# Kernel tuning notes

Measured on AMD Instinct MI355X. Metric: run time of the kernel, lower is better.

The kernel has to match this reference:

```python
import jax, jax.numpy as jnp
import numpy as np

HIDDEN = 128

def setup_inputs() -> dict:
    key = jax.random.key(0)
    ks = jax.random.split(key, 4)
    B, T, D, H = 64, 2048, 64, HIDDEN
    scale_ih = 1.0 / np.sqrt(D)
    scale_hh = 1.0 / np.sqrt(H)
    return {
        "input_data": jax.random.normal(ks[0], (B, T, D), dtype=jnp.float32),
        "W_ih": jax.random.normal(ks[1], (4 * H, D), dtype=jnp.float32) * scale_ih,
        "W_hh": jax.random.normal(ks[2], (4 * H, H), dtype=jnp.float32) * scale_hh,
        "b_ih": jnp.zeros((4 * H,), dtype=jnp.float32),
        "b_hh": jnp.zeros((4 * H,), dtype=jnp.float32),
        "h0": jnp.zeros((B, H), dtype=jnp.float32),
        "c0": jnp.zeros((B, H), dtype=jnp.float32),
    }

def reference(input_data, W_ih, W_hh, b_ih, b_hh, h0, c0):
    # Single-layer LSTM over the sequence, PyTorch gate order (i, f, g, o).
    H = h0.shape[-1]
    b = b_ih + b_hh  # (4H,)
    # Precompute input projections for all timesteps: (T, B, 4H)
    x_proj = jnp.einsum('btd,gd->tbg', input_data, W_ih) + b

    def step(carry, xp_t):
        h, c = carry  # (B, H) each
        gates = xp_t + h @ W_hh.T  # (B, 4H)
        i = jax.nn.sigmoid(gates[:, 0 * H:1 * H])
        f = jax.nn.sigmoid(gates[:, 1 * H:2 * H])
        g = jnp.tanh(gates[:, 2 * H:3 * H])
        o = jax.nn.sigmoid(gates[:, 3 * H:4 * H])
        c_new = f * c + i * g
        h_new = o * jnp.tanh(c_new)
        return (h_new, c_new), h_new

    (_, _), hs = jax.lax.scan(step, (h0, c0), x_proj)  # hs: (T, B, H)
    input_encoded = jnp.transpose(hs, (1, 0, 2))  # (B, T, H)
    return input_encoded
```

## Files before the change

### kernel.cpp

```cpp
#include <hip/hip_runtime.h>

typedef _Float16 half2f __attribute__((ext_vector_type(2)));

#define HID 128
#define G4  512
#define DIN 64

__device__ __forceinline__ float fdot2(half2f a, half2f b, float c) {
  return __builtin_amdgcn_fdot2(a, b, c, false);
}
__device__ __forceinline__ half2f as_h2(unsigned int u) {
  return __builtin_bit_cast(half2f, u);
}
__device__ __forceinline__ half2f mk2(float a, float b) {
  half2f r; r.x = (_Float16)a; r.y = (_Float16)b; return r;
}
__device__ __forceinline__ float sigmoidf_fast(float x) {
  return __builtin_amdgcn_rcpf(1.0f + __expf(-x));
}
__device__ __forceinline__ float tanhf_fast(float x) {
  return 2.0f * __builtin_amdgcn_rcpf(1.0f + __expf(-2.0f * x)) - 1.0f;
}
template <int CTRL>
__device__ __forceinline__ float dpp_add(float x) {
  int m = __builtin_amdgcn_update_dpp(0, __builtin_bit_cast(int, x),
                                      CTRL, 0xF, 0xF, true);
  return x + __builtin_bit_cast(float, m);
}
#define QP_XOR1 0xB1

__device__ __forceinline__ void barrier_lgkm() {
  asm volatile("s_waitcnt lgkmcnt(0)" ::: "memory");
  __builtin_amdgcn_s_barrier();
  asm volatile("" ::: "memory");
}

__global__ __launch_bounds__(512, 2)
void xproj_kernel(const float* __restrict__ x, const float* __restrict__ Wih,
                  const float* __restrict__ bih, const float* __restrict__ bhh,
                  _Float16* __restrict__ xp, int nrows)
{
  const int gp   = threadIdx.x;
  const int unit = gp >> 2;
  const int gate = gp & 3;
  const int row  = gate * HID + unit;

  half2f wi[32];
  {
    const float4* wr = (const float4*)(Wih + (size_t)row * DIN);
#pragma unroll
    for (int q = 0; q < 16; q++) {
      float4 v = wr[q];
      wi[2 * q + 0] = mk2(v.x, v.y);
      wi[2 * q + 1] = mk2(v.z, v.w);
    }
  }
  const float bias = bih[row] + bhh[row];

  __shared__ __align__(16) _Float16 xin[8 * DIN];

  const int rows_per_block = (nrows + (int)gridDim.x - 1) / (int)gridDim.x;
  const int r0 = blockIdx.x * rows_per_block;
  const int r1 = (r0 + rows_per_block < nrows) ? (r0 + rows_per_block) : nrows;

  const int rsub = threadIdx.x >> 6;
  const int dd   = threadIdx.x & 63;

  float vld = 0.f;
  if (r0 + rsub < nrows) vld = x[(size_t)(r0 + rsub) * DIN + dd];

  for (int r = r0; r < r1; r += 8) {
    barrier_lgkm();
    xin[rsub * DIN + dd] = (_Float16)vld;
    barrier_lgkm();
    int rn = r + 8 + rsub;
    if (rn < nrows) vld = x[(size_t)rn * DIN + dd];

    const uint4* xi4 = (const uint4*)xin;
#pragma unroll
    for (int k = 0; k < 8; k++) {
      if (r + k >= r1) break;
      const uint4* rowp = xi4 + k * (DIN / 8);
      float a[4] = {bias, 0.f, 0.f, 0.f};
#pragma unroll
      for (int q = 0; q < 8; q++) {
        uint4 hv = rowp[q];
        a[q & 3] = fdot2(as_h2(hv.x), wi[4 * q + 0], a[q & 3]);
        a[q & 3] = fdot2(as_h2(hv.y), wi[4 * q + 1], a[q & 3]);
        a[q & 3] = fdot2(as_h2(hv.z), wi[4 * q + 2], a[q & 3]);
        a[q & 3] = fdot2(as_h2(hv.w), wi[4 * q + 3], a[q & 3]);
      }
      xp[(size_t)(r + k) * G4 + gp] = (_Float16)(a[0] + a[1] + a[2] + a[3]);
    }
  }
}

__global__ __launch_bounds__(256, 1)
void lstm_scan5(const float* __restrict__ Whh,
                const float* __restrict__ h0, const float* __restrict__ c0,
                const _Float16* __restrict__ xp,
                float* __restrict__ out, int T)
{
  const int tid = threadIdx.x;
  const int j   = tid >> 1;
  const int kq  = tid & 1;
  const int b   = blockIdx.x;

  half2f w0[32], w1[32], w2[32], w3[32];
  {
    const float4* r0 = (const float4*)(Whh + ((size_t)(0 * HID + j)) * HID + kq * 64);
    const float4* r1 = (const float4*)(Whh + ((size_t)(1 * HID + j)) * HID + kq * 64);
    const float4* r2 = (const float4*)(Whh + ((size_t)(2 * HID + j)) * HID + kq * 64);
    const float4* r3 = (const float4*)(Whh + ((size_t)(3 * HID + j)) * HID + kq * 64);
#pragma unroll
    for (int q = 0; q < 16; q++) {
      float4 v;
      v = r0[q]; w0[2 * q] = mk2(v.x, v.y); w0[2 * q + 1] = mk2(v.z, v.w);
      v = r1[q]; w1[2 * q] = mk2(v.x, v.y); w1[2 * q + 1] = mk2(v.z, v.w);
      v = r2[q]; w2[2 * q] = mk2(v.x, v.y); w2[2 * q + 1] = mk2(v.z, v.w);
      v = r3[q]; w3[2 * q] = mk2(v.x, v.y); w3[2 * q + 1] = mk2(v.z, v.w);
    }
  }

  __shared__ __align__(16) _Float16 h_sh[2][HID];

  float c = c0[(size_t)b * HID + j];
  if (kq == 0) h_sh[0][j] = (_Float16)h0[(size_t)b * HID + j];
  __syncthreads();

  const unsigned int* xp32 = (const unsigned int*)xp;
  const size_t xbase = (size_t)b * T * 256 + (size_t)j * 2 + kq;
  unsigned int xv  = xp32[xbase];
  unsigned int xv1 = (T > 1) ? xp32[xbase + 256] : 0u;

  const _Float16* rb = h_sh[0];
  _Float16*       wb = h_sh[1];

  for (int t = 0; t < T; ++t) {
    unsigned int xv2 = 0;
    if (t + 2 < T) xv2 = xp32[xbase + (size_t)(t + 2) * 256];

    uint4 hv[8];
    const uint4* h4 = (const uint4*)(rb + kq * 64);
#pragma unroll
    for (int q = 0; q < 8; q++) hv[q] = h4[q];

    float a0 = 0.f, a1 = 0.f, a2 = 0.f, a3 = 0.f;
#pragma unroll
    for (int q = 0; q < 8; q++) {
      unsigned int d0 = hv[q].x, d1 = hv[q].y, d2 = hv[q].z, d3 = hv[q].w;
      a0 = fdot2(as_h2(d0), w0[4 * q + 0], a0);
      a1 = fdot2(as_h2(d0), w1[4 * q + 0], a1);
      a2 = fdot2(as_h2(d0), w2[4 * q + 0], a2);
      a3 = fdot2(as_h2(d0), w3[4 * q + 0], a3);
      a0 = fdot2(as_h2(d1), w0[4 * q + 1], a0);
      a1 = fdot2(as_h2(d1), w1[4 * q + 1], a1);
      a2 = fdot2(as_h2(d1), w2[4 * q + 1], a2);
      a3 = fdot2(as_h2(d1), w3[4 * q + 1], a3);
      a0 = fdot2(as_h2(d2), w0[4 * q + 2], a0);
      a1 = fdot2(as_h2(d2), w1[4 * q + 2], a1);
      a2 = fdot2(as_h2(d2), w2[4 * q + 2], a2);
      a3 = fdot2(as_h2(d2), w3[4 * q + 2], a3);
      a0 = fdot2(as_h2(d3), w0[4 * q + 3], a0);
      a1 = fdot2(as_h2(d3), w1[4 * q + 3], a1);
      a2 = fdot2(as_h2(d3), w2[4 * q + 3], a2);
      a3 = fdot2(as_h2(d3), w3[4 * q + 3], a3);
    }

    {
      half2f xh = as_h2(xv);
      float x0 = (float)xh.x, x1 = (float)xh.y;
      if (kq == 0) { a0 += x0; a1 += x1; }
      else         { a2 += x0; a3 += x1; }
    }

    a0 = dpp_add<QP_XOR1>(a0);
    a1 = dpp_add<QP_XOR1>(a1);
    a2 = dpp_add<QP_XOR1>(a2);
    a3 = dpp_add<QP_XOR1>(a3);

    float i  = sigmoidf_fast(a0);
    float f  = sigmoidf_fast(a1);
    float gg = tanhf_fast(a2);
    float o  = sigmoidf_fast(a3);
    c = f * c + i * gg;
    float h = o * tanhf_fast(c);

    if (kq == 0) {
      wb[j] = (_Float16)h;
      out[((size_t)b * T + t) * HID + j] = h;
    }
    barrier_lgkm();
    const _Float16* tmp = rb; rb = wb; wb = (_Float16*)tmp;
    xv = xv1; xv1 = xv2;
  }
}

__global__ __launch_bounds__(512, 2)
void lstm_scan_fb(const float* __restrict__ x, const float* __restrict__ Wih,
                  const float* __restrict__ Whh,
                  const float* __restrict__ bih, const float* __restrict__ bhh,
                  const float* __restrict__ h0, const float* __restrict__ c0,
                  float* __restrict__ out, int T)
{
  const int g = threadIdx.x;
  const int b = blockIdx.x;

  half2f w[64];
  {
    const float4* wr = (const float4*)(Whh + (size_t)g * HID);
#pragma unroll
    for (int q = 0; q < 32; q++) {
      float4 v = wr[q];
      w[2 * q + 0] = mk2(v.x, v.y);
      w[2 * q + 1] = mk2(v.z, v.w);
    }
  }
  half2f wi[32];
  float bias;
  {
    const float4* wr = (const float4*)(Wih + (size_t)g * DIN);
#pragma unroll
    for (int q = 0; q < 16; q++) {
      float4 v = wr[q];
      wi[2 * q + 0] = mk2(v.x, v.y);
      wi[2 * q + 1] = mk2(v.z, v.w);
    }
    bias = bih[g] + bhh[g];
  }

  __shared__ __align__(16) _Float16 h_sh[HID];
  __shared__ __align__(16) _Float16 xin[DIN];
  __shared__ float pre[G4];

  float c = 0.f;
  if (g < HID) {
    c = c0[(size_t)b * HID + g];
    h_sh[g] = (_Float16)h0[(size_t)b * HID + g];
  }
  if (g < DIN) xin[g] = (_Float16)x[((size_t)b * T) * DIN + g];
  __syncthreads();

  const bool is_tanh_gate = (g >= 2 * HID) && (g < 3 * HID);

  for (int t = 0; t < T; ++t) {
    float a[4] = {0.f, 0.f, 0.f, 0.f};
    const uint4* h4 = (const uint4*)h_sh;
#pragma unroll
    for (int q = 0; q < 16; q++) {
      uint4 hv = h4[q];
      a[q & 3] = fdot2(as_h2(hv.x), w[4 * q + 0], a[q & 3]);
      a[q & 3] = fdot2(as_h2(hv.y), w[4 * q + 1], a[q & 3]);
      a[q & 3] = fdot2(as_h2(hv.z), w[4 * q + 2], a[q & 3]);
      a[q & 3] = fdot2(as_h2(hv.w), w[4 * q + 3], a[q & 3]);
    }
    const uint4* x4 = (const uint4*)xin;
#pragma unroll
    for (int q = 0; q < 8; q++) {
      uint4 hv = x4[q];
      a[q & 3] = fdot2(as_h2(hv.x), wi[4 * q + 0], a[q & 3]);
      a[q & 3] = fdot2(as_h2(hv.y), wi[4 * q + 1], a[q & 3]);
      a[q & 3] = fdot2(as_h2(hv.z), wi[4 * q + 2], a[q & 3]);
      a[q & 3] = fdot2(as_h2(hv.w), wi[4 * q + 3], a[q & 3]);
    }
    float preact = a[0] + a[1] + a[2] + a[3] + bias;
    float act = is_tanh_gate ? tanhf_fast(preact) : sigmoidf_fast(preact);
    pre[g] = act;
    __syncthreads();

    if (g < HID) {
      float i  = pre[g];
      float f  = pre[g + HID];
      float gg = pre[g + 2 * HID];
      float o  = pre[g + 3 * HID];
      c = f * c + i * gg;
      float h = o * tanhf_fast(c);
      out[((size_t)b * T + t) * HID + g] = h;
      h_sh[g] = (_Float16)h;
    } else if (g >= HID && g < HID + DIN) {
      int d = g - HID;
      if (t + 1 < T) xin[d] = (_Float16)x[((size_t)b * T + (t + 1)) * DIN + d];
    }
    __syncthreads();
  }
}

extern "C" void kernel_launch(void* const* d_in, const int* in_sizes, int n_in,
                              void* d_out, int out_size, void* d_ws, size_t ws_size,
                              hipStream_t stream)
{
  const float* x   = (const float*)d_in[0];
  const float* Wih = (const float*)d_in[1];
  const float* Whh = (const float*)d_in[2];
  const float* bih = (const float*)d_in[3];
  const float* bhh = (const float*)d_in[4];
  const float* h0  = (const float*)d_in[5];
  const float* c0  = (const float*)d_in[6];
  float* out = (float*)d_out;

  const int B = in_sizes[5] / HID;
  const int T = in_sizes[0] / (B * DIN);
  const int nrows = B * T;

  const size_t xp_bytes = (size_t)nrows * G4 * sizeof(_Float16);
  if (ws_size >= xp_bytes) {
    _Float16* xp = (_Float16*)d_ws;
    xproj_kernel<<<1024, 512, 0, stream>>>(x, Wih, bih, bhh, xp, nrows);
    lstm_scan5<<<B, 256, 0, stream>>>(Whh, h0, c0, xp, out, T);
  } else {
    lstm_scan_fb<<<B, 512, 0, stream>>>(x, Wih, Whh, bih, bhh, h0, c0, out, T);
  }
}
```

Before: 1.092 ms.

## Use MFMA 16x16x32 for recurrent matvec with permuted x-projection layout

The per-timestep h·W_hh^T product, previously done with fdot2 per thread, now runs on MFMA 16x16x32 f16 instructions. Each wave holds W_hh fragments in registers, and the x-projection is written in a permuted order so one uint4 load per lane seeds the accumulators. Gate activations are computed per lane with a unified sigmoid/tanh formula and broadcast with DPP quad permutes. The MFMA uses only one useful row of the 16-row A tile, so most of its work is wasted; this shortens the serial dependency chain per step in exchange for that waste and a more complex lane mapping.

```diff
diff --git a/kernel.cpp b/kernel.cpp
--- a/kernel.cpp
+++ b/kernel.cpp
@@ -1,6 +1,8 @@
 #include <hip/hip_runtime.h>
 
 typedef _Float16 half2f __attribute__((ext_vector_type(2)));
+typedef _Float16 half8  __attribute__((ext_vector_type(8)));
+typedef float    floatx4 __attribute__((ext_vector_type(4)));
 
 #define HID 128
 #define G4  512
@@ -15,6 +17,14 @@
 __device__ __forceinline__ half2f mk2(float a, float b) {
   half2f r; r.x = (_Float16)a; r.y = (_Float16)b; return r;
 }
+__device__ __forceinline__ half8 cvt8(float4 a, float4 b) {
+  half8 r;
+  r[0] = (_Float16)a.x; r[1] = (_Float16)a.y;
+  r[2] = (_Float16)a.z; r[3] = (_Float16)a.w;
+  r[4] = (_Float16)b.x; r[5] = (_Float16)b.y;
+  r[6] = (_Float16)b.z; r[7] = (_Float16)b.w;
+  return r;
+}
 __device__ __forceinline__ float sigmoidf_fast(float x) {
   return __builtin_amdgcn_rcpf(1.0f + __expf(-x));
 }
@@ -22,12 +32,15 @@
   return 2.0f * __builtin_amdgcn_rcpf(1.0f + __expf(-2.0f * x)) - 1.0f;
 }
 template <int CTRL>
-__device__ __forceinline__ float dpp_add(float x) {
+__device__ __forceinline__ float dpp_bcast(float x) {
   int m = __builtin_amdgcn_update_dpp(0, __builtin_bit_cast(int, x),
                                       CTRL, 0xF, 0xF, true);
-  return x + __builtin_bit_cast(float, m);
-}
-#define QP_XOR1 0xB1
+  return __builtin_bit_cast(float, m);
+}
+#define QP_B0 0x00
+#define QP_B1 0x55
+#define QP_B2 0xAA
+#define QP_B3 0xFF
 
 __device__ __forceinline__ void barrier_lgkm() {
   asm volatile("s_waitcnt lgkmcnt(0)" ::: "memory");
@@ -44,6 +57,7 @@
   const int unit = gp >> 2;
   const int gate = gp & 3;
   const int row  = gate * HID + unit;
+  const int sidx = ((gp >> 7) << 7) + ((gp & 15) << 3) + ((gp >> 4) & 7);
 
   half2f wi[32];
   {
@@ -90,109 +104,129 @@
         a[q & 3] = fdot2(as_h2(hv.z), wi[4 * q + 2], a[q & 3]);
         a[q & 3] = fdot2(as_h2(hv.w), wi[4 * q + 3], a[q & 3]);
       }
-      xp[(size_t)(r + k) * G4 + gp] = (_Float16)(a[0] + a[1] + a[2] + a[3]);
+      xp[(size_t)(r + k) * G4 + sidx] = (_Float16)(a[0] + a[1] + a[2] + a[3]);
     }
   }
 }
 
 __global__ __launch_bounds__(256, 1)
-void lstm_scan5(const float* __restrict__ Whh,
+void lstm_scan6(const float* __restrict__ Whh,
                 const float* __restrict__ h0, const float* __restrict__ c0,
                 const _Float16* __restrict__ xp,
                 float* __restrict__ out, int T)
 {
-  const int tid = threadIdx.x;
-  const int j   = tid >> 1;
-  const int kq  = tid & 1;
-  const int b   = blockIdx.x;
-
-  half2f w0[32], w1[32], w2[32], w3[32];
-  {
-    const float4* r0 = (const float4*)(Whh + ((size_t)(0 * HID + j)) * HID + kq * 64);
-    const float4* r1 = (const float4*)(Whh + ((size_t)(1 * HID + j)) * HID + kq * 64);
-    const float4* r2 = (const float4*)(Whh + ((size_t)(2 * HID + j)) * HID + kq * 64);
-    const float4* r3 = (const float4*)(Whh + ((size_t)(3 * HID + j)) * HID + kq * 64);
-#pragma unroll
-    for (int q = 0; q < 16; q++) {
-      float4 v;
-      v = r0[q]; w0[2 * q] = mk2(v.x, v.y); w0[2 * q + 1] = mk2(v.z, v.w);
-      v = r1[q]; w1[2 * q] = mk2(v.x, v.y); w1[2 * q + 1] = mk2(v.z, v.w);
-      v = r2[q]; w2[2 * q] = mk2(v.x, v.y); w2[2 * q + 1] = mk2(v.z, v.w);
-      v = r3[q]; w3[2 * q] = mk2(v.x, v.y); w3[2 * q + 1] = mk2(v.z, v.w);
-    }
-  }
+  const int tid  = threadIdx.x;
+  const int w    = tid >> 6;
+  const int lane = tid & 63;
+  const int s    = lane >> 4;
+  const int col  = lane & 15;
+  const int gt   = lane & 3;
+  const int b    = blockIdx.x;
+
+  half8 bfr[8][4];
+#pragma unroll
+  for (int ti = 0; ti < 8; ti++) {
+    const int G    = (w * 8 + ti) * 16 + col;
+    const int unit = G >> 2;
+    const int g_   = G & 3;
+    const float* wrow = Whh + (size_t)(g_ * HID + unit) * HID;
+#pragma unroll
+    for (int kc = 0; kc < 4; kc++) {
+      const float4* p = (const float4*)(wrow + kc * 32 + s * 8);
+      bfr[ti][kc] = cvt8(p[0], p[1]);
+    }
+  }
+
+  const float kk = (gt == 2) ? -2.f : -1.f;
+  const float mm = (gt == 2) ?  2.f :  1.f;
+  const float bb = (gt == 2) ? -1.f :  0.f;
+
+  const int u0 = w * 32 + s * 8 + (col >> 2);
+  const int u1 = u0 + 4;
 
   __shared__ __align__(16) _Float16 h_sh[2][HID];
 
-  float c = c0[(size_t)b * HID + j];
-  if (kq == 0) h_sh[0][j] = (_Float16)h0[(size_t)b * HID + j];
-  __syncthreads();
-
-  const unsigned int* xp32 = (const unsigned int*)xp;
-  const size_t xbase = (size_t)b * T * 256 + (size_t)j * 2 + kq;
-  unsigned int xv  = xp32[xbase];
-  unsigned int xv1 = (T > 1) ? xp32[xbase + 256] : 0u;
+  float cA = c0[(size_t)b * HID + u0];
+  float cB = c0[(size_t)b * HID + u1];
+  if (tid < HID) h_sh[0][tid] = (_Float16)h0[(size_t)b * HID + tid];
+
+  const uint4* xp4 = (const uint4*)xp;
+  const size_t xbase = (size_t)b * T * (G4 / 8) + w * 16 + col;
+  uint4 xq  = xp4[xbase];
+  uint4 xq1 = (T > 1) ? xp4[xbase + 64] : xq;
+
+  barrier_lgkm();
 
   const _Float16* rb = h_sh[0];
   _Float16*       wb = h_sh[1];
 
   for (int t = 0; t < T; ++t) {
-    unsigned int xv2 = 0;
-    if (t + 2 < T) xv2 = xp32[xbase + (size_t)(t + 2) * 256];
-
-    uint4 hv[8];
-    const uint4* h4 = (const uint4*)(rb + kq * 64);
-#pragma unroll
-    for (int q = 0; q < 8; q++) hv[q] = h4[q];
-
-    float a0 = 0.f, a1 = 0.f, a2 = 0.f, a3 = 0.f;
-#pragma unroll
-    for (int q = 0; q < 8; q++) {
-      unsigned int d0 = hv[q].x, d1 = hv[q].y, d2 = hv[q].z, d3 = hv[q].w;
-      a0 = fdot2(as_h2(d0), w0[4 * q + 0], a0);
-      a1 = fdot2(as_h2(d0), w1[4 * q + 0], a1);
-      a2 = fdot2(as_h2(d0), w2[4 * q + 0], a2);
-      a3 = fdot2(as_h2(d0), w3[4 * q + 0], a3);
-      a0 = fdot2(as_h2(d1), w0[4 * q + 1], a0);
-      a1 = fdot2(as_h2(d1), w1[4 * q + 1], a1);
-      a2 = fdot2(as_h2(d1), w2[4 * q + 1], a2);
-      a3 = fdot2(as_h2(d1), w3[4 * q + 1], a3);
-      a0 = fdot2(as_h2(d2), w0[4 * q + 2], a0);
-      a1 = fdot2(as_h2(d2), w1[4 * q + 2], a1);
-      a2 = fdot2(as_h2(d2), w2[4 * q + 2], a2);
-      a3 = fdot2(as_h2(d2), w3[4 * q + 2], a3);
-      a0 = fdot2(as_h2(d3), w0[4 * q + 3], a0);
-      a1 = fdot2(as_h2(d3), w1[4 * q + 3], a1);
-      a2 = fdot2(as_h2(d3), w2[4 * q + 3], a2);
-      a3 = fdot2(as_h2(d3), w3[4 * q + 3], a3);
-    }
-
-    {
-      half2f xh = as_h2(xv);
-      float x0 = (float)xh.x, x1 = (float)xh.y;
-      if (kq == 0) { a0 += x0; a1 += x1; }
-      else         { a2 += x0; a3 += x1; }
-    }
-
-    a0 = dpp_add<QP_XOR1>(a0);
-    a1 = dpp_add<QP_XOR1>(a1);
-    a2 = dpp_add<QP_XOR1>(a2);
-    a3 = dpp_add<QP_XOR1>(a3);
-
-    float i  = sigmoidf_fast(a0);
-    float f  = sigmoidf_fast(a1);
-    float gg = tanhf_fast(a2);
-    float o  = sigmoidf_fast(a3);
-    c = f * c + i * gg;
-    float h = o * tanhf_fast(c);
-
-    if (kq == 0) {
-      wb[j] = (_Float16)h;
-      out[((size_t)b * T + t) * HID + j] = h;
-    }
+    uint4 xq2 = xq1;
+    if (t + 2 < T) xq2 = xp4[xbase + (size_t)(t + 2) * 64];
+
+    const uint4* h4 = (const uint4*)rb;
+    half8 af0 = __builtin_bit_cast(half8, h4[0 * 4 + s]);
+    half8 af1 = __builtin_bit_cast(half8, h4[1 * 4 + s]);
+    half8 af2 = __builtin_bit_cast(half8, h4[2 * 4 + s]);
+    half8 af3 = __builtin_bit_cast(half8, h4[3 * 4 + s]);
+
+    half8 xh = __builtin_bit_cast(half8, xq);
+    floatx4 acc[8];
+#pragma unroll
+    for (int ti = 0; ti < 8; ti++) {
+      float xv = (float)xh[ti];
+      acc[ti] = (floatx4){xv, xv, xv, xv};
+    }
+
+#pragma unroll
+    for (int ti = 0; ti < 8; ti++)
+      acc[ti] = __builtin_amdgcn_mfma_f32_16x16x32_f16(af0, bfr[ti][0], acc[ti], 0, 0, 0);
+#pragma unroll
+    for (int ti = 0; ti < 8; ti++)
+      acc[ti] = __builtin_amdgcn_mfma_f32_16x16x32_f16(af1, bfr[ti][1], acc[ti], 0, 0, 0);
+#pragma unroll
+    for (int ti = 0; ti < 8; ti++)
+      acc[ti] = __builtin_amdgcn_mfma_f32_16x16x32_f16(af2, bfr[ti][2], acc[ti], 0, 0, 0);
+#pragma unroll
+    for (int ti = 0; ti < 8; ti++)
+      acc[ti] = __builtin_amdgcn_mfma_f32_16x16x32_f16(af3, bfr[ti][3], acc[ti], 0, 0, 0);
+
+    float e0 = (s & 1) ? acc[2][0] : acc[0][0];
+    float e1 = (s & 1) ? acc[6][0] : acc[4][0];
+    float vA = (s & 2) ? e1 : e0;
+    float o0 = (s & 1) ? acc[3][0] : acc[1][0];
+    float o1 = (s & 1) ? acc[7][0] : acc[5][0];
+    float vB = (s & 2) ? o1 : o0;
+
+    float actA = fmaf(mm, __builtin_amdgcn_rcpf(1.0f + __expf(kk * vA)), bb);
+    float actB = fmaf(mm, __builtin_amdgcn_rcpf(1.0f + __expf(kk * vB)), bb);
+
+    float giA = dpp_bcast<QP_B0>(actA);
+    float gfA = dpp_bcast<QP_B1>(actA);
+    float ggA = dpp_bcast<QP_B2>(actA);
+    float goA = dpp_bcast<QP_B3>(actA);
+    float giB = dpp_bcast<QP_B0>(actB);
+    float gfB = dpp_bcast<QP_B1>(actB);
+    float ggB = dpp_bcast<QP_B2>(actB);
+    float goB = dpp_bcast<QP_B3>(actB);
+
+    cA = fmaf(gfA, cA, giA * ggA);
+    cB = fmaf(gfB, cB, giB * ggB);
+    float hA = goA * tanhf_fast(cA);
+    float hB = goB * tanhf_fast(cB);
+
+    if (gt == 0) {
+      wb[u0] = (_Float16)hA;
+      wb[u1] = (_Float16)hB;
+    } else if (gt == 1) {
+      const size_t obase = ((size_t)b * T + t) * HID;
+      out[obase + u0] = hA;
+      out[obase + u1] = hB;
+    }
+
     barrier_lgkm();
     const _Float16* tmp = rb; rb = wb; wb = (_Float16*)tmp;
-    xv = xv1; xv1 = xv2;
+    xq = xq1; xq1 = xq2;
   }
 }
 
@@ -306,7 +340,7 @@
   if (ws_size >= xp_bytes) {
     _Float16* xp = (_Float16*)d_ws;
     xproj_kernel<<<1024, 512, 0, stream>>>(x, Wih, bih, bhh, xp, nrows);
-    lstm_scan5<<<B, 256, 0, stream>>>(Whh, h0, c0, xp, out, T);
+    lstm_scan6<<<B, 256, 0, stream>>>(Whh, h0, c0, xp, out, T);
   } else {
     lstm_scan_fb<<<B, 512, 0, stream>>>(x, Wih, Whh, bih, bhh, h0, c0, out, T);
   }
```

Result: slower. 1.332 ms (+22.0%).
